# Kernel tuning notes

Measured on AMD Instinct MI355X. Metric: run time of the kernel, lower is better.

Reference implementation:

```python
import jax, jax.numpy as jnp
import numpy as np

SLICES = [(12, 1), (13, 1)]  # (input_width, hidden_size=1) per slice


def _lstm_last_hidden(xs, W_ih, W_hh, b):
    """Run a standard (PyTorch gate order i,f,g,o) LSTM over time, return last h.
    xs: [T, B, in]; W_ih: [4*H, in]; W_hh: [4*H, H]; b: [4*H] (b_ih + b_hh).
    Returns h_T: [B, H].
    """
    B = xs.shape[1]
    H = W_hh.shape[1]
    h0 = jnp.zeros((B, H), xs.dtype)
    c0 = jnp.zeros((B, H), xs.dtype)

    def step(carry, xt):
        h, c = carry
        gates = xt @ W_ih.T + h @ W_hh.T + b  # [B, 4H]
        i, f, g, o = jnp.split(gates, 4, axis=-1)
        i = jax.nn.sigmoid(i)
        f = jax.nn.sigmoid(f)
        g = jnp.tanh(g)
        o = jax.nn.sigmoid(o)
        c = f * c + i * g
        h = o * jnp.tanh(c)
        return (h, c), None

    (hT, _), _ = jax.lax.scan(step, (h0, c0), xs)
    return hT


def setup_inputs() -> dict:
    key = jax.random.key(0)
    ks = jax.random.split(key, 9)
    B, T, F = 4096, 512, 25
    nb_out = 1
    s = 0.1
    x = jax.random.normal(ks[0], (B, T, F), dtype=jnp.float32)
    # slice-1 LSTM (input 12, hidden 1)
    W_ih1 = jax.random.normal(ks[1], (4, 12), dtype=jnp.float32) * s
    W_hh1 = jax.random.normal(ks[2], (4, 1), dtype=jnp.float32) * s
    b1 = jax.random.normal(ks[3], (4,), dtype=jnp.float32) * s
    # slice-2 LSTM (input 13, hidden 1)
    W_ih2 = jax.random.normal(ks[4], (4, 13), dtype=jnp.float32) * s
    W_hh2 = jax.random.normal(ks[5], (4, 1), dtype=jnp.float32) * s
    b2 = jax.random.normal(ks[6], (4,), dtype=jnp.float32) * s
    # output head Linear(2, nb_out)
    W_out = jax.random.normal(ks[7], (nb_out, 2), dtype=jnp.float32) * s
    b_out = jax.random.normal(ks[8], (nb_out,), dtype=jnp.float32) * s
    return {"x": x, "W_ih1": W_ih1, "W_hh1": W_hh1, "b1": b1,
            "W_ih2": W_ih2, "W_hh2": W_hh2, "b2": b2,
            "W_out": W_out, "b_out": b_out}


def reference(x, W_ih1, W_hh1, b1, W_ih2, W_hh2, b2, W_out, b_out):
    # x: [B, T, 25] -> time-major [T, B, 25]
    xs = jnp.transpose(x, (1, 0, 2))
    h1 = _lstm_last_hidden(xs[..., :12], W_ih1, W_hh1, b1)   # [B, 1]
    h2 = _lstm_last_hidden(xs[..., 12:], W_ih2, W_hh2, b2)   # [B, 1]
    h = jnp.concatenate([h1, h2], axis=-1)                   # [B, 2] == lstm_out[:, -1, :]
    out = h @ W_out.T + b_out                                # [B, nb_out]
    return jax.nn.sigmoid(out)
```

## Files before the change

kernel.cpp:

```cpp
#include <hip/hip_runtime.h>
#include <stdint.h>


#define T_STEPS 512
#define F_IN    25
#define TC      32
#define NT1     (T_STEPS / TC)
#define CH      8
#define TILE_F  (CH * TC * F_IN)
#define LOG2E   1.44269504088896340736f
#define SC1     (-LOG2E)
#define SC2     (-2.0f * LOG2E)

typedef const __attribute__((address_space(1))) void* as1_cvp;
typedef __attribute__((address_space(3)))       void* as3_vp;

__device__ __forceinline__ void gll16(const float* gsrc, const float* ldst) {
  __builtin_amdgcn_global_load_lds((as1_cvp)(uintptr_t)gsrc,
                                   (as3_vp)(uint32_t)(uintptr_t)ldst, 16, 0, 0);
}

__global__ void __launch_bounds__(256, 2)
k1_gates(const float* __restrict__ x,
         const float* __restrict__ Wih1, const float* __restrict__ b1,
         const float* __restrict__ Wih2, const float* __restrict__ b2,
         float* __restrict__ z, int B)
{
  __shared__ __align__(16) float xs[2 * TILE_F];

  const int tid  = threadIdx.x;
  const int wv   = tid >> 6;
  const int lane = tid & 63;
  const int b0   = blockIdx.x * CH;

  const float* gp[7];
  int ioff[7];
#pragma unroll
  for (int j = 0; j < 7; ++j) {
    const int i = wv + 4 * j;
    if (i < 25) {
      const int F = i * 256 + lane * 4;
      const int c = F / (TC * F_IN);
      const int r = F - c * (TC * F_IN);
      gp[j]   = x + (size_t)(b0 + c) * (T_STEPS * F_IN) + r;
      ioff[j] = i * 256;
    } else { gp[j] = x; ioff[j] = -1; }
  }

  const int c  = tid >> 5;
  const int tl = tid & 31;

#pragma unroll
  for (int j = 0; j < 7; ++j)
    if (ioff[j] >= 0) gll16(gp[j], xs + ioff[j]);
  __syncthreads();

  float4* __restrict__ z4 = (float4*)z;

  for (int k = 0; k < NT1; ++k) {
    if (k + 1 < NT1) {
      const int h = (k + 1) & 1;
#pragma unroll
      for (int j = 0; j < 7; ++j)
        if (ioff[j] >= 0) gll16(gp[j] + (k + 1) * (TC * F_IN), xs + h * TILE_F + ioff[j]);
    }

    const float* xr = xs + (k & 1) * TILE_F + c * (TC * F_IN) + tl * F_IN;
    float zz[8];
#pragma unroll
    for (int j = 0; j < 4; ++j) { zz[j] = b1[j]; zz[4 + j] = b2[j]; }
#pragma unroll
    for (int f = 0; f < 12; ++f) {
      const float xv = xr[f];
#pragma unroll
      for (int j = 0; j < 4; ++j) zz[j] = fmaf(Wih1[j * 12 + f], xv, zz[j]);
    }
#pragma unroll
    for (int f = 0; f < 13; ++f) {
      const float xv = xr[12 + f];
#pragma unroll
      for (int j = 0; j < 4; ++j) zz[4 + j] = fmaf(Wih2[j * 13 + f], xv, zz[4 + j]);
    }
    const float4 q0 = make_float4(zz[0] * SC1, zz[1] * SC1, zz[2] * SC2, zz[3] * SC1);
    const float4 q1 = make_float4(zz[4] * SC1, zz[5] * SC1, zz[6] * SC2, zz[7] * SC1);
    const size_t idx = (size_t)(k * TC + tl) * B + (b0 + c);
    z4[idx * 2]     = q0;
    z4[idx * 2 + 1] = q1;

    __syncthreads();
  }
}

__device__ __forceinline__ void lstm_step(const float4 zv,
                                          const float wi, const float wf,
                                          const float wg, const float wo,
                                          float& h, float& cc) {
  const float ei = __builtin_amdgcn_exp2f(fmaf(h, wi, zv.x));
  const float ef = __builtin_amdgcn_exp2f(fmaf(h, wf, zv.y));
  const float eg = __builtin_amdgcn_exp2f(fmaf(h, wg, zv.z));
  const float eo = __builtin_amdgcn_exp2f(fmaf(h, wo, zv.w));
  const float af  = __builtin_amdgcn_rcpf(1.0f + ef);
  const float rig = __builtin_amdgcn_rcpf((1.0f + ei) * (1.0f + eg));
  const float ig  = (1.0f - eg) * rig;
  cc = fmaf(af, cc, ig);
  const float ec  = __builtin_amdgcn_exp2f(cc * SC2);
  const float roc = __builtin_amdgcn_rcpf((1.0f + eo) * (1.0f + ec));
  h = (1.0f - ec) * roc;
}

__global__ void __launch_bounds__(64, 1)
k2_scan(const float* __restrict__ z,
        const float* __restrict__ Whh1, const float* __restrict__ Whh2,
        const float* __restrict__ Wout, const float* __restrict__ bout,
        float* __restrict__ out, int B)
{
  const int l    = threadIdx.x;
  const int bb   = blockIdx.x * 32 + (l >> 1);
  const int lstm = l & 1;

  const float* wp = lstm ? Whh2 : Whh1;
  const float wi = SC1 * wp[0];
  const float wf = SC1 * wp[1];
  const float wg = SC2 * wp[2];
  const float wo = SC1 * wp[3];

  const float4* __restrict__ zp = (const float4*)z;
  const size_t stride = (size_t)B * 2;
  const size_t base   = (size_t)bb * 2 + lstm;

  float4 rb[8];
#pragma unroll
  for (int j = 0; j < 8; ++j) rb[j] = zp[(size_t)j * stride + base];

  float h = 0.0f, cc = 0.0f;

  for (int t0 = 0; t0 < T_STEPS - 8; t0 += 8) {
#pragma unroll
    for (int j = 0; j < 8; ++j) {
      lstm_step(rb[j], wi, wf, wg, wo, h, cc);
      rb[j] = zp[(size_t)(t0 + j + 8) * stride + base];
    }
  }
#pragma unroll
  for (int j = 0; j < 8; ++j) lstm_step(rb[j], wi, wf, wg, wo, h, cc);

  const float hp = __shfl_xor(h, 1);
  if (lstm == 0) {
    const float p = fmaf(Wout[0], h, fmaf(Wout[1], hp, bout[0]));
    out[bb] = __builtin_amdgcn_rcpf(1.0f + __builtin_amdgcn_exp2f(p * SC1));
  }
}

extern "C" void kernel_launch(void* const* d_in, const int* in_sizes, int n_in,
                              void* d_out, int out_size, void* d_ws, size_t ws_size,
                              hipStream_t stream) {
  const float* x    = (const float*)d_in[0];
  const float* Wih1 = (const float*)d_in[1];
  const float* Whh1 = (const float*)d_in[2];
  const float* b1   = (const float*)d_in[3];
  const float* Wih2 = (const float*)d_in[4];
  const float* Whh2 = (const float*)d_in[5];
  const float* b2   = (const float*)d_in[6];
  const float* Wout = (const float*)d_in[7];
  const float* bout = (const float*)d_in[8];
  float* out = (float*)d_out;
  float* z   = (float*)d_ws;

  const int B = in_sizes[0] / (T_STEPS * F_IN);

  hipLaunchKernelGGL(k1_gates, dim3(B / CH), dim3(256), 0, stream,
                     x, Wih1, b1, Wih2, b2, z, B);
  hipLaunchKernelGGL(k2_scan, dim3(B / 32), dim3(64), 0, stream,
                     z, Whh1, Whh2, Wout, bout, out, B);
}
```

Measured before the change: 349.1 us.

## Store gate preactivations as fp16 and load x directly without LDS staging

The intermediate gate buffer z is stored as packed half2 (8 halves per batch-timestep) instead of float, halving the write traffic of k1 and the read traffic of the sequential scan kernel. k1 drops the async global-to-LDS double buffering and has each thread load its 25 inputs straight from global memory, with the log2e scaling folded into register-resident weights. The scan kernel now issues the next prefetch before computing. The fp16 rounding of preactivations adds numerical error that accumulates over 512 recurrent steps, and the direct per-thread strided loads may coalesce worse than the LDS path.

```diff
diff --git a/kernel.cpp b/kernel.cpp
--- a/kernel.cpp
+++ b/kernel.cpp
@@ -1,104 +1,87 @@
 #include <hip/hip_runtime.h>
+#include <hip/hip_fp16.h>
 #include <stdint.h>
 
 
 #define T_STEPS 512
 #define F_IN    25
-#define TC      32
-#define NT1     (T_STEPS / TC)
 #define CH      8
-#define TILE_F  (CH * TC * F_IN)
 #define LOG2E   1.44269504088896340736f
 #define SC1     (-LOG2E)
 #define SC2     (-2.0f * LOG2E)
-
-typedef const __attribute__((address_space(1))) void* as1_cvp;
-typedef __attribute__((address_space(3)))       void* as3_vp;
-
-__device__ __forceinline__ void gll16(const float* gsrc, const float* ldst) {
-  __builtin_amdgcn_global_load_lds((as1_cvp)(uintptr_t)gsrc,
-                                   (as3_vp)(uint32_t)(uintptr_t)ldst, 16, 0, 0);
-}
 
 __global__ void __launch_bounds__(256, 2)
 k1_gates(const float* __restrict__ x,
          const float* __restrict__ Wih1, const float* __restrict__ b1,
          const float* __restrict__ Wih2, const float* __restrict__ b2,
-         float* __restrict__ z, int B)
+         uint4* __restrict__ z, int B)
 {
-  __shared__ __align__(16) float xs[2 * TILE_F];
+  const int tid = threadIdx.x;
+  const int c   = tid & 7;
+  const int tl  = tid >> 3;
+  const int b   = blockIdx.x * CH + c;
 
-  const int tid  = threadIdx.x;
-  const int wv   = tid >> 6;
-  const int lane = tid & 63;
-  const int b0   = blockIdx.x * CH;
-
-  const float* gp[7];
-  int ioff[7];
+  float w1[48], w2[52], bb[8];
 #pragma unroll
-  for (int j = 0; j < 7; ++j) {
-    const int i = wv + 4 * j;
-    if (i < 25) {
-      const int F = i * 256 + lane * 4;
-      const int c = F / (TC * F_IN);
-      const int r = F - c * (TC * F_IN);
-      gp[j]   = x + (size_t)(b0 + c) * (T_STEPS * F_IN) + r;
-      ioff[j] = i * 256;
-    } else { gp[j] = x; ioff[j] = -1; }
+  for (int j = 0; j < 4; ++j) {
+    const float s = (j == 2) ? SC2 : SC1;
+#pragma unroll
+    for (int f = 0; f < 12; ++f) w1[j * 12 + f] = Wih1[j * 12 + f] * s;
+#pragma unroll
+    for (int f = 0; f < 13; ++f) w2[j * 13 + f] = Wih2[j * 13 + f] * s;
+    bb[j]     = b1[j] * s;
+    bb[4 + j] = b2[j] * s;
   }
 
-  const int c  = tid >> 5;
-  const int tl = tid & 31;
+  const float* __restrict__ xrow = x + (size_t)b * (T_STEPS * F_IN);
 
+  for (int k = 0; k < T_STEPS / 32; ++k) {
+    const int t = k * 32 + tl;
+    const float* __restrict__ xr = xrow + t * F_IN;
+
+    float xv[25];
 #pragma unroll
-  for (int j = 0; j < 7; ++j)
-    if (ioff[j] >= 0) gll16(gp[j], xs + ioff[j]);
-  __syncthreads();
+    for (int f = 0; f < 25; ++f) xv[f] = xr[f];
 
-  float4* __restrict__ z4 = (float4*)z;
-
-  for (int k = 0; k < NT1; ++k) {
-    if (k + 1 < NT1) {
-      const int h = (k + 1) & 1;
-#pragma unroll
-      for (int j = 0; j < 7; ++j)
-        if (ioff[j] >= 0) gll16(gp[j] + (k + 1) * (TC * F_IN), xs + h * TILE_F + ioff[j]);
-    }
-
-    const float* xr = xs + (k & 1) * TILE_F + c * (TC * F_IN) + tl * F_IN;
     float zz[8];
 #pragma unroll
-    for (int j = 0; j < 4; ++j) { zz[j] = b1[j]; zz[4 + j] = b2[j]; }
+    for (int j = 0; j < 8; ++j) zz[j] = bb[j];
 #pragma unroll
     for (int f = 0; f < 12; ++f) {
-      const float xv = xr[f];
 #pragma unroll
-      for (int j = 0; j < 4; ++j) zz[j] = fmaf(Wih1[j * 12 + f], xv, zz[j]);
+      for (int j = 0; j < 4; ++j) zz[j] = fmaf(w1[j * 12 + f], xv[f], zz[j]);
     }
 #pragma unroll
     for (int f = 0; f < 13; ++f) {
-      const float xv = xr[12 + f];
 #pragma unroll
-      for (int j = 0; j < 4; ++j) zz[4 + j] = fmaf(Wih2[j * 13 + f], xv, zz[4 + j]);
+      for (int j = 0; j < 4; ++j) zz[4 + j] = fmaf(w2[j * 13 + f], xv[12 + f], zz[4 + j]);
     }
-    const float4 q0 = make_float4(zz[0] * SC1, zz[1] * SC1, zz[2] * SC2, zz[3] * SC1);
-    const float4 q1 = make_float4(zz[4] * SC1, zz[5] * SC1, zz[6] * SC2, zz[7] * SC1);
-    const size_t idx = (size_t)(k * TC + tl) * B + (b0 + c);
-    z4[idx * 2]     = q0;
-    z4[idx * 2 + 1] = q1;
 
-    __syncthreads();
+    const __half2 p0 = __floats2half2_rn(zz[0], zz[1]);
+    const __half2 p1 = __floats2half2_rn(zz[2], zz[3]);
+    const __half2 p2 = __floats2half2_rn(zz[4], zz[5]);
+    const __half2 p3 = __floats2half2_rn(zz[6], zz[7]);
+    uint4 q;
+    q.x = *(const unsigned int*)&p0;
+    q.y = *(const unsigned int*)&p1;
+    q.z = *(const unsigned int*)&p2;
+    q.w = *(const unsigned int*)&p3;
+    z[(size_t)t * B + b] = q;
   }
 }
 
-__device__ __forceinline__ void lstm_step(const float4 zv,
+__device__ __forceinline__ void lstm_step(const uint2 v,
                                           const float wi, const float wf,
                                           const float wg, const float wo,
                                           float& h, float& cc) {
-  const float ei = __builtin_amdgcn_exp2f(fmaf(h, wi, zv.x));
-  const float ef = __builtin_amdgcn_exp2f(fmaf(h, wf, zv.y));
-  const float eg = __builtin_amdgcn_exp2f(fmaf(h, wg, zv.z));
-  const float eo = __builtin_amdgcn_exp2f(fmaf(h, wo, zv.w));
+  const __half2 h01 = *(const __half2*)&v.x;
+  const __half2 h23 = *(const __half2*)&v.y;
+  const float2 f01 = __half22float2(h01);
+  const float2 f23 = __half22float2(h23);
+  const float ei = __builtin_amdgcn_exp2f(fmaf(h, wi, f01.x));
+  const float ef = __builtin_amdgcn_exp2f(fmaf(h, wf, f01.y));
+  const float eg = __builtin_amdgcn_exp2f(fmaf(h, wg, f23.x));
+  const float eo = __builtin_amdgcn_exp2f(fmaf(h, wo, f23.y));
   const float af  = __builtin_amdgcn_rcpf(1.0f + ef);
   const float rig = __builtin_amdgcn_rcpf((1.0f + ei) * (1.0f + eg));
   const float ig  = (1.0f - eg) * rig;
@@ -109,7 +92,7 @@
 }
 
 __global__ void __launch_bounds__(64, 1)
-k2_scan(const float* __restrict__ z,
+k2_scan(const uint2* __restrict__ z,
         const float* __restrict__ Whh1, const float* __restrict__ Whh2,
         const float* __restrict__ Wout, const float* __restrict__ bout,
         float* __restrict__ out, int B)
@@ -124,21 +107,21 @@
   const float wg = SC2 * wp[2];
   const float wo = SC1 * wp[3];
 
-  const float4* __restrict__ zp = (const float4*)z;
+  const uint2* __restrict__ zp = z + (size_t)bb * 2 + lstm;
   const size_t stride = (size_t)B * 2;
-  const size_t base   = (size_t)bb * 2 + lstm;
 
-  float4 rb[8];
+  uint2 rb[8];
 #pragma unroll
-  for (int j = 0; j < 8; ++j) rb[j] = zp[(size_t)j * stride + base];
+  for (int j = 0; j < 8; ++j) rb[j] = zp[(size_t)j * stride];
 
   float h = 0.0f, cc = 0.0f;
 
   for (int t0 = 0; t0 < T_STEPS - 8; t0 += 8) {
 #pragma unroll
     for (int j = 0; j < 8; ++j) {
-      lstm_step(rb[j], wi, wf, wg, wo, h, cc);
-      rb[j] = zp[(size_t)(t0 + j + 8) * stride + base];
+      const uint2 v = rb[j];
+      rb[j] = zp[(size_t)(t0 + j + 8) * stride];
+      lstm_step(v, wi, wf, wg, wo, h, cc);
     }
   }
 #pragma unroll
@@ -164,12 +147,11 @@
   const float* Wout = (const float*)d_in[7];
   const float* bout = (const float*)d_in[8];
   float* out = (float*)d_out;
-  float* z   = (float*)d_ws;
 
   const int B = in_sizes[0] / (T_STEPS * F_IN);
 
   hipLaunchKernelGGL(k1_gates, dim3(B / CH), dim3(256), 0, stream,
-                     x, Wih1, b1, Wih2, b2, z, B);
+                     x, Wih1, b1, Wih2, b2, (uint4*)d_ws, B);
   hipLaunchKernelGGL(k2_scan, dim3(B / 32), dim3(64), 0, stream,
-                     z, Whh1, Whh2, Wout, bout, out, B);
+                     (const uint2*)d_ws, Whh1, Whh2, Wout, bout, out, B);
 }
```

Measured after the change: 344.6 us. About the same (-1.3%).
